# Performance work log

Hardware: AMD Instinct MI355X
Metric: run time of the kernel (lower is better)

## Reference

```python
import jax, jax.numpy as jnp
import numpy as np

B, T, D_IN, H, D_OUT = 4096, 512, 10, 20, 2


def setup_inputs() -> dict:
    key = jax.random.key(0)
    ks = jax.random.split(key, 12)
    s = 1.0 / np.sqrt(H)  # PyTorch-style uniform bound scale (use normal*s)
    return {
        "x": jax.random.normal(ks[0], (B, T, D_IN), jnp.float32),
        "w_ih0": jax.random.normal(ks[1], (H, D_IN), jnp.float32) * s,
        "w_hh0": jax.random.normal(ks[2], (H, H), jnp.float32) * s,
        "b_ih0": jax.random.normal(ks[3], (H,), jnp.float32) * s,
        "b_hh0": jax.random.normal(ks[4], (H,), jnp.float32) * s,
        "w_ih1": jax.random.normal(ks[5], (H, H), jnp.float32) * s,
        "w_hh1": jax.random.normal(ks[6], (H, H), jnp.float32) * s,
        "b_ih1": jax.random.normal(ks[7], (H,), jnp.float32) * s,
        "b_hh1": jax.random.normal(ks[8], (H,), jnp.float32) * s,
        "fc_w": jax.random.normal(ks[9], (D_OUT, H), jnp.float32) * s,
        "fc_b": jax.random.normal(ks[10], (D_OUT,), jnp.float32) * s,
    }


def _rnn_layer(inp, w_ih, w_hh, b_ih, b_hh):
    # inp: [B, T, Din]. Precompute input projection once (batched GEMM),
    # then scan the sequential recurrence: h_t = tanh(x_t W_ih^T + b_ih + h_{t-1} W_hh^T + b_hh)
    xp = jnp.einsum('btd,hd->bth', inp, w_ih) + (b_ih + b_hh)  # [B, T, H]

    def step(h, xt):
        h = jnp.tanh(xt + h @ w_hh.T)
        return h, h

    h0 = jnp.zeros((inp.shape[0], w_hh.shape[0]), inp.dtype)
    _, hs = jax.lax.scan(step, h0, jnp.swapaxes(xp, 0, 1))  # hs: [T, B, H]
    return jnp.swapaxes(hs, 0, 1)  # [B, T, H]


def reference(x, w_ih0, w_hh0, b_ih0, b_hh0, w_ih1, w_hh1, b_ih1, b_hh1, fc_w, fc_b):
    h1 = _rnn_layer(x, w_ih0, w_hh0, b_ih0, b_hh0)
    h2 = _rnn_layer(h1, w_ih1, w_hh1, b_ih1, b_hh1)
    last = h2[:, -1, :]  # [B, H]
    return last @ fc_w.T + fc_b  # [B, D_OUT]
```

## Files before the change

### kernel.cpp

```cpp
#include <hip/hip_runtime.h>
#include <cstdint>

constexpr int B_   = 4096;
constexpr int T_   = 512;
constexpr int DIN  = 10;
constexpr int H_   = 20;
constexpr int DOUT = 2;

constexpr int SPW = 3;
constexpr int CH  = 2;
constexpr int XV  = CH * DIN / 4;

#define CFENCE() asm volatile("" ::: "memory")

__device__ __forceinline__ float fast_tanh(float v) {
    float e = __builtin_amdgcn_exp2f(v * 2.885390082f );
    float r = __builtin_amdgcn_rcpf(e + 1.0f);
    return fmaf(-2.0f, r, 1.0f);
}

extern "C" __global__ void __launch_bounds__(64, 2)
rnn_fused(const float* __restrict__ x,
          const float* __restrict__ w_ih0, const float* __restrict__ w_hh0,
          const float* __restrict__ b_ih0, const float* __restrict__ b_hh0,
          const float* __restrict__ w_ih1, const float* __restrict__ w_hh1,
          const float* __restrict__ b_ih1, const float* __restrict__ b_hh1,
          const float* __restrict__ fc_w, const float* __restrict__ fc_b,
          float* __restrict__ out)
{
    const int lane = threadIdx.x;
    const int sl   = lane / H_;
    const int i    = lane - sl * H_;
    const int samp = blockIdx.x * SPW + sl;
    const int sc   = (samp < B_) ? samp : (B_ - 1);
    const int slc  = (sl < SPW) ? sl : SPW;

    __shared__ __align__(16) float h1s[SPW + 1][H_];
    __shared__ __align__(16) float h2s[SPW + 1][H_];

    float wi0[DIN];
    {
        const float2* p = reinterpret_cast<const float2*>(w_ih0 + i * DIN);
        #pragma unroll
        for (int k = 0; k < DIN / 2; ++k) {
            float2 v = p[k];
            wi0[2 * k] = v.x; wi0[2 * k + 1] = v.y;
        }
    }
    float wh0[H_], wi1[H_], wh1[H_];
    {
        const float4* p0 = reinterpret_cast<const float4*>(w_hh0 + i * H_);
        const float4* p1 = reinterpret_cast<const float4*>(w_ih1 + i * H_);
        const float4* p2 = reinterpret_cast<const float4*>(w_hh1 + i * H_);
        #pragma unroll
        for (int k = 0; k < H_ / 4; ++k) {
            float4 a = p0[k]; wh0[4*k]=a.x; wh0[4*k+1]=a.y; wh0[4*k+2]=a.z; wh0[4*k+3]=a.w;
            float4 b = p1[k]; wi1[4*k]=b.x; wi1[4*k+1]=b.y; wi1[4*k+2]=b.z; wi1[4*k+3]=b.w;
            float4 c = p2[k]; wh1[4*k]=c.x; wh1[4*k+1]=c.y; wh1[4*k+2]=c.z; wh1[4*k+3]=c.w;
        }
    }
    const float bias0 = b_ih0[i] + b_hh0[i];
    const float bias1 = b_ih1[i] + b_hh1[i];

    float h1[H_], h2[H_];
    #pragma unroll
    for (int j = 0; j < H_; ++j) { h1[j] = 0.0f; h2[j] = 0.0f; }

    const float4* xb = reinterpret_cast<const float4*>(x + (size_t)sc * (T_ * DIN));

    float4 xv[XV];
    #pragma unroll
    for (int k = 0; k < XV; ++k) xv[k] = xb[k];

    for (int t0 = 0; t0 < T_; t0 += CH) {
        float xp[CH];
        #pragma unroll
        for (int m = 0; m < CH; ++m) xp[m] = bias0;
        #pragma unroll
        for (int k = 0; k < XV; ++k) {
            int idx = 4 * k;
            xp[(idx+0)/DIN] = fmaf(xv[k].x, wi0[(idx+0)%DIN], xp[(idx+0)/DIN]);
            xp[(idx+1)/DIN] = fmaf(xv[k].y, wi0[(idx+1)%DIN], xp[(idx+1)/DIN]);
            xp[(idx+2)/DIN] = fmaf(xv[k].z, wi0[(idx+2)%DIN], xp[(idx+2)/DIN]);
            xp[(idx+3)/DIN] = fmaf(xv[k].w, wi0[(idx+3)%DIN], xp[(idx+3)/DIN]);
        }

        {
            const int t0n = (t0 + CH < T_) ? (t0 + CH) : 0;
            #pragma unroll
            for (int k = 0; k < XV; ++k) xv[k] = xb[(t0n * DIN) / 4 + k];
        }

        #pragma unroll
        for (int m = 0; m < CH; ++m) {
            float a0 = xp[m], a1 = 0.f, a2 = 0.f, a3 = 0.f;
            #pragma unroll
            for (int j = 0; j < H_; j += 4) {
                a0 = fmaf(h1[j+0], wh0[j+0], a0);
                a1 = fmaf(h1[j+1], wh0[j+1], a1);
                a2 = fmaf(h1[j+2], wh0[j+2], a2);
                a3 = fmaf(h1[j+3], wh0[j+3], a3);
            }
            float h1n = fast_tanh((a0 + a1) + (a2 + a3));

            CFENCE();
            h1s[slc][i] = h1n;
            CFENCE();

            float b0 = bias1, b1 = 0.f, b2 = 0.f, b3 = 0.f;
            #pragma unroll
            for (int j = 0; j < H_; j += 4) {
                b0 = fmaf(h2[j+0], wh1[j+0], b0);
                b1 = fmaf(h2[j+1], wh1[j+1], b1);
                b2 = fmaf(h2[j+2], wh1[j+2], b2);
                b3 = fmaf(h2[j+3], wh1[j+3], b3);
            }

            #pragma unroll
            for (int k = 0; k < H_ / 4; ++k) {
                float4 v = reinterpret_cast<const float4*>(&h1s[slc][0])[k];
                h1[4*k]=v.x; h1[4*k+1]=v.y; h1[4*k+2]=v.z; h1[4*k+3]=v.w;
            }
            CFENCE();

            #pragma unroll
            for (int j = 0; j < H_; j += 4) {
                b0 = fmaf(h1[j+0], wi1[j+0], b0);
                b1 = fmaf(h1[j+1], wi1[j+1], b1);
                b2 = fmaf(h1[j+2], wi1[j+2], b2);
                b3 = fmaf(h1[j+3], wi1[j+3], b3);
            }
            float h2n = fast_tanh((b0 + b1) + (b2 + b3));

            CFENCE();
            h2s[slc][i] = h2n;
            CFENCE();
            #pragma unroll
            for (int k = 0; k < H_ / 4; ++k) {
                float4 v = reinterpret_cast<const float4*>(&h2s[slc][0])[k];
                h2[4*k]=v.x; h2[4*k+1]=v.y; h2[4*k+2]=v.z; h2[4*k+3]=v.w;
            }
            CFENCE();
        }
    }

    if (sl < SPW && samp < B_ && i < DOUT) {
        float acc = fc_b[i];
        #pragma unroll
        for (int j = 0; j < H_; ++j) acc = fmaf(h2[j], fc_w[i * H_ + j], acc);
        out[samp * DOUT + i] = acc;
    }
}

extern "C" void kernel_launch(void* const* d_in, const int* in_sizes, int n_in,
                              void* d_out, int out_size, void* d_ws, size_t ws_size,
                              hipStream_t stream) {
    (void)in_sizes; (void)n_in; (void)d_ws; (void)ws_size; (void)out_size;
    const float* x     = (const float*)d_in[0];
    const float* w_ih0 = (const float*)d_in[1];
    const float* w_hh0 = (const float*)d_in[2];
    const float* b_ih0 = (const float*)d_in[3];
    const float* b_hh0 = (const float*)d_in[4];
    const float* w_ih1 = (const float*)d_in[5];
    const float* w_hh1 = (const float*)d_in[6];
    const float* b_ih1 = (const float*)d_in[7];
    const float* b_hh1 = (const float*)d_in[8];
    const float* fc_w  = (const float*)d_in[9];
    const float* fc_b  = (const float*)d_in[10];
    float* out = (float*)d_out;

    const int grid = (B_ + SPW - 1) / SPW;
    hipLaunchKernelGGL(rnn_fused, dim3(grid), dim3(64), 0, stream,
                       x, w_ih0, w_hh0, b_ih0, b_hh0,
                       w_ih1, w_hh1, b_ih1, b_hh1, fc_w, fc_b, out);
}
```

Baseline: 167.9 us.

## Split RNN layers across two wavefronts with a barrier-synchronised layer pipeline

Each block now runs two wavefronts. Wave 0 computes layer 0 and writes h1 into a double-buffered shared array, and wave 1 consumes it one step behind to compute layer 1. The two waves synchronise with a block barrier every timestep. The goal is to shorten the serial dependency chain per wave and let the two layers run concurrently. The cost is a barrier per step and more threads per sample group, which may reduce how many sample groups fit per CU. The input chunk size also grows from 2 to 4 timesteps.

```diff
diff --git a/kernel.cpp b/kernel.cpp
--- a/kernel.cpp
+++ b/kernel.cpp
@@ -8,105 +8,137 @@
 constexpr int DOUT = 2;
 
 constexpr int SPW = 3;
-constexpr int CH  = 2;
+constexpr int CH  = 4;
 constexpr int XV  = CH * DIN / 4;
 
 #define CFENCE() asm volatile("" ::: "memory")
+#define LGKM0()  asm volatile("s_waitcnt lgkmcnt(0)" ::: "memory")
+#define BAR()    do { CFENCE(); __builtin_amdgcn_s_barrier(); CFENCE(); } while (0)
 
 __device__ __forceinline__ float fast_tanh(float v) {
-    float e = __builtin_amdgcn_exp2f(v * 2.885390082f );
+    float e = __builtin_amdgcn_exp2f(v * 2.885390082f);
     float r = __builtin_amdgcn_rcpf(e + 1.0f);
     return fmaf(-2.0f, r, 1.0f);
 }
 
-extern "C" __global__ void __launch_bounds__(64, 2)
-rnn_fused(const float* __restrict__ x,
-          const float* __restrict__ w_ih0, const float* __restrict__ w_hh0,
-          const float* __restrict__ b_ih0, const float* __restrict__ b_hh0,
-          const float* __restrict__ w_ih1, const float* __restrict__ w_hh1,
-          const float* __restrict__ b_ih1, const float* __restrict__ b_hh1,
-          const float* __restrict__ fc_w, const float* __restrict__ fc_b,
-          float* __restrict__ out)
+extern "C" __global__ void __launch_bounds__(128, 2)
+rnn_pipe(const float* __restrict__ x,
+         const float* __restrict__ w_ih0, const float* __restrict__ w_hh0,
+         const float* __restrict__ b_ih0, const float* __restrict__ b_hh0,
+         const float* __restrict__ w_ih1, const float* __restrict__ w_hh1,
+         const float* __restrict__ b_ih1, const float* __restrict__ b_hh1,
+         const float* __restrict__ fc_w, const float* __restrict__ fc_b,
+         float* __restrict__ out)
 {
-    const int lane = threadIdx.x;
+    const int tid  = threadIdx.x;
+    const int wv   = tid >> 6;
+    const int lane = tid & 63;
     const int sl   = lane / H_;
     const int i    = lane - sl * H_;
     const int samp = blockIdx.x * SPW + sl;
     const int sc   = (samp < B_) ? samp : (B_ - 1);
     const int slc  = (sl < SPW) ? sl : SPW;
 
-    __shared__ __align__(16) float h1s[SPW + 1][H_];
+    __shared__ __align__(16) float h1s[2][SPW + 1][H_];
     __shared__ __align__(16) float h2s[SPW + 1][H_];
 
-    float wi0[DIN];
-    {
-        const float2* p = reinterpret_cast<const float2*>(w_ih0 + i * DIN);
+    if (wv == 0) {
+        float wi0[DIN];
+        {
+            const float2* p = reinterpret_cast<const float2*>(w_ih0 + i * DIN);
+            #pragma unroll
+            for (int k = 0; k < DIN / 2; ++k) { float2 v = p[k]; wi0[2*k] = v.x; wi0[2*k+1] = v.y; }
+        }
+        float wh0[H_];
+        {
+            const float4* p = reinterpret_cast<const float4*>(w_hh0 + i * H_);
+            #pragma unroll
+            for (int k = 0; k < H_ / 4; ++k) {
+                float4 v = p[k]; wh0[4*k]=v.x; wh0[4*k+1]=v.y; wh0[4*k+2]=v.z; wh0[4*k+3]=v.w;
+            }
+        }
+        const float bias0 = b_ih0[i] + b_hh0[i];
+
+        float h1[H_];
         #pragma unroll
-        for (int k = 0; k < DIN / 2; ++k) {
-            float2 v = p[k];
-            wi0[2 * k] = v.x; wi0[2 * k + 1] = v.y;
-        }
-    }
-    float wh0[H_], wi1[H_], wh1[H_];
-    {
-        const float4* p0 = reinterpret_cast<const float4*>(w_hh0 + i * H_);
-        const float4* p1 = reinterpret_cast<const float4*>(w_ih1 + i * H_);
-        const float4* p2 = reinterpret_cast<const float4*>(w_hh1 + i * H_);
-        #pragma unroll
-        for (int k = 0; k < H_ / 4; ++k) {
-            float4 a = p0[k]; wh0[4*k]=a.x; wh0[4*k+1]=a.y; wh0[4*k+2]=a.z; wh0[4*k+3]=a.w;
-            float4 b = p1[k]; wi1[4*k]=b.x; wi1[4*k+1]=b.y; wi1[4*k+2]=b.z; wi1[4*k+3]=b.w;
-            float4 c = p2[k]; wh1[4*k]=c.x; wh1[4*k+1]=c.y; wh1[4*k+2]=c.z; wh1[4*k+3]=c.w;
-        }
-    }
-    const float bias0 = b_ih0[i] + b_hh0[i];
-    const float bias1 = b_ih1[i] + b_hh1[i];
-
-    float h1[H_], h2[H_];
-    #pragma unroll
-    for (int j = 0; j < H_; ++j) { h1[j] = 0.0f; h2[j] = 0.0f; }
-
-    const float4* xb = reinterpret_cast<const float4*>(x + (size_t)sc * (T_ * DIN));
-
-    float4 xv[XV];
-    #pragma unroll
-    for (int k = 0; k < XV; ++k) xv[k] = xb[k];
-
-    for (int t0 = 0; t0 < T_; t0 += CH) {
-        float xp[CH];
-        #pragma unroll
-        for (int m = 0; m < CH; ++m) xp[m] = bias0;
+        for (int j = 0; j < H_; ++j) h1[j] = 0.0f;
+
+        const float4* xb = reinterpret_cast<const float4*>(x + (size_t)sc * (T_ * DIN));
+        float xf[4 * XV];
         #pragma unroll
         for (int k = 0; k < XV; ++k) {
-            int idx = 4 * k;
-            xp[(idx+0)/DIN] = fmaf(xv[k].x, wi0[(idx+0)%DIN], xp[(idx+0)/DIN]);
-            xp[(idx+1)/DIN] = fmaf(xv[k].y, wi0[(idx+1)%DIN], xp[(idx+1)/DIN]);
-            xp[(idx+2)/DIN] = fmaf(xv[k].z, wi0[(idx+2)%DIN], xp[(idx+2)/DIN]);
-            xp[(idx+3)/DIN] = fmaf(xv[k].w, wi0[(idx+3)%DIN], xp[(idx+3)/DIN]);
-        }
-
+            float4 v = xb[k];
+            xf[4*k]=v.x; xf[4*k+1]=v.y; xf[4*k+2]=v.z; xf[4*k+3]=v.w;
+        }
+
+        #pragma unroll 1
+        for (int t0 = 0; t0 < T_; t0 += CH) {
+            float xp[CH];
+            #pragma unroll
+            for (int m = 0; m < CH; ++m) {
+                float s0 = bias0, s1 = 0.0f;
+                #pragma unroll
+                for (int d = 0; d < DIN; d += 2) {
+                    s0 = fmaf(xf[m*DIN + d],     wi0[d],     s0);
+                    s1 = fmaf(xf[m*DIN + d + 1], wi0[d + 1], s1);
+                }
+                xp[m] = s0 + s1;
+            }
+            {
+                const int t0n  = (t0 + CH < T_) ? (t0 + CH) : 0;
+                const int base = t0n * DIN / 4;
+                #pragma unroll
+                for (int k = 0; k < XV; ++k) {
+                    float4 v = xb[base + k];
+                    xf[4*k]=v.x; xf[4*k+1]=v.y; xf[4*k+2]=v.z; xf[4*k+3]=v.w;
+                }
+            }
+            #pragma unroll
+            for (int m = 0; m < CH; ++m) {
+                const int p = m & 1;
+                float a0 = xp[m], a1 = 0.f, a2 = 0.f, a3 = 0.f;
+                #pragma unroll
+                for (int j = 0; j < H_; j += 4) {
+                    a0 = fmaf(h1[j+0], wh0[j+0], a0);
+                    a1 = fmaf(h1[j+1], wh0[j+1], a1);
+                    a2 = fmaf(h1[j+2], wh0[j+2], a2);
+                    a3 = fmaf(h1[j+3], wh0[j+3], a3);
+                }
+                float h1n = fast_tanh((a0 + a1) + (a2 + a3));
+                CFENCE();
+                h1s[p][slc][i] = h1n;
+                LGKM0();
+                #pragma unroll
+                for (int k = 0; k < H_ / 4; ++k) {
+                    float4 v = reinterpret_cast<const float4*>(&h1s[p][slc][0])[k];
+                    h1[4*k]=v.x; h1[4*k+1]=v.y; h1[4*k+2]=v.z; h1[4*k+3]=v.w;
+                }
+                CFENCE();
+                BAR();
+            }
+        }
+        BAR();
+    } else {
+        float wi1[H_], wh1[H_];
         {
-            const int t0n = (t0 + CH < T_) ? (t0 + CH) : 0;
-            #pragma unroll
-            for (int k = 0; k < XV; ++k) xv[k] = xb[(t0n * DIN) / 4 + k];
-        }
-
+            const float4* p1 = reinterpret_cast<const float4*>(w_ih1 + i * H_);
+            const float4* p2 = reinterpret_cast<const float4*>(w_hh1 + i * H_);
+            #pragma unroll
+            for (int k = 0; k < H_ / 4; ++k) {
+                float4 a = p1[k]; wi1[4*k]=a.x; wi1[4*k+1]=a.y; wi1[4*k+2]=a.z; wi1[4*k+3]=a.w;
+                float4 b = p2[k]; wh1[4*k]=b.x; wh1[4*k+1]=b.y; wh1[4*k+2]=b.z; wh1[4*k+3]=b.w;
+            }
+        }
+        const float bias1 = b_ih1[i] + b_hh1[i];
+        float h2[H_];
         #pragma unroll
-        for (int m = 0; m < CH; ++m) {
-            float a0 = xp[m], a1 = 0.f, a2 = 0.f, a3 = 0.f;
-            #pragma unroll
-            for (int j = 0; j < H_; j += 4) {
-                a0 = fmaf(h1[j+0], wh0[j+0], a0);
-                a1 = fmaf(h1[j+1], wh0[j+1], a1);
-                a2 = fmaf(h1[j+2], wh0[j+2], a2);
-                a3 = fmaf(h1[j+3], wh0[j+3], a3);
-            }
-            float h1n = fast_tanh((a0 + a1) + (a2 + a3));
-
-            CFENCE();
-            h1s[slc][i] = h1n;
-            CFENCE();
-
+        for (int j = 0; j < H_; ++j) h2[j] = 0.0f;
+
+        BAR();
+
+        #pragma unroll 2
+        for (int t = 0; t < T_; ++t) {
+            const int p = t & 1;
             float b0 = bias1, b1 = 0.f, b2 = 0.f, b3 = 0.f;
             #pragma unroll
             for (int j = 0; j < H_; j += 4) {
@@ -115,23 +147,20 @@
                 b2 = fmaf(h2[j+2], wh1[j+2], b2);
                 b3 = fmaf(h2[j+3], wh1[j+3], b3);
             }
-
-            #pragma unroll
-            for (int k = 0; k < H_ / 4; ++k) {
-                float4 v = reinterpret_cast<const float4*>(&h1s[slc][0])[k];
-                h1[4*k]=v.x; h1[4*k+1]=v.y; h1[4*k+2]=v.z; h1[4*k+3]=v.w;
-            }
-            CFENCE();
-
+            float h1v[H_];
+            #pragma unroll
+            for (int k = 0; k < H_ / 4; ++k) {
+                float4 v = reinterpret_cast<const float4*>(&h1s[p][slc][0])[k];
+                h1v[4*k]=v.x; h1v[4*k+1]=v.y; h1v[4*k+2]=v.z; h1v[4*k+3]=v.w;
+            }
             #pragma unroll
             for (int j = 0; j < H_; j += 4) {
-                b0 = fmaf(h1[j+0], wi1[j+0], b0);
-                b1 = fmaf(h1[j+1], wi1[j+1], b1);
-                b2 = fmaf(h1[j+2], wi1[j+2], b2);
-                b3 = fmaf(h1[j+3], wi1[j+3], b3);
+                b0 = fmaf(h1v[j+0], wi1[j+0], b0);
+                b1 = fmaf(h1v[j+1], wi1[j+1], b1);
+                b2 = fmaf(h1v[j+2], wi1[j+2], b2);
+                b3 = fmaf(h1v[j+3], wi1[j+3], b3);
             }
             float h2n = fast_tanh((b0 + b1) + (b2 + b3));
-
             CFENCE();
             h2s[slc][i] = h2n;
             CFENCE();
@@ -141,14 +170,15 @@
                 h2[4*k]=v.x; h2[4*k+1]=v.y; h2[4*k+2]=v.z; h2[4*k+3]=v.w;
             }
             CFENCE();
-        }
-    }
-
-    if (sl < SPW && samp < B_ && i < DOUT) {
-        float acc = fc_b[i];
-        #pragma unroll
-        for (int j = 0; j < H_; ++j) acc = fmaf(h2[j], fc_w[i * H_ + j], acc);
-        out[samp * DOUT + i] = acc;
+            BAR();
+        }
+
+        if (sl < SPW && samp < B_ && i < DOUT) {
+            float acc = fc_b[i];
+            #pragma unroll
+            for (int j = 0; j < H_; ++j) acc = fmaf(h2[j], fc_w[i * H_ + j], acc);
+            out[samp * DOUT + i] = acc;
+        }
     }
 }
 
@@ -170,7 +200,7 @@
     float* out = (float*)d_out;
 
     const int grid = (B_ + SPW - 1) / SPW;
-    hipLaunchKernelGGL(rnn_fused, dim3(grid), dim3(64), 0, stream,
+    hipLaunchKernelGGL(rnn_pipe, dim3(grid), dim3(128), 0, stream,
                        x, w_ih0, w_hh0, b_ih0, b_hh0,
                        w_ih1, w_hh1, b_ih1, b_hh1, fc_w, fc_b, out);
 }
```

After: 196.9 us. +17.3%, slower.
